# Kernel tuning notes

Hardware: AMD Instinct MI355X
Metric: run time of the kernel (lower is better)

## Reference

```python
import jax, jax.numpy as jnp
import numpy as np

B, S, V, E, H, K = 64, 512, 50000, 128, 256, 20
PAD_IDX, SOS_IDX = 0, 19
NEG = -9999.0


def _lstm_dir(x, mask, W_ih, W_hh, b):
    # x: [B,S,E], mask: [B,S] float. PyTorch gate order: i,f,g,o.
    xg = jnp.einsum('bse,ge->bsg', x, W_ih) + b  # [B,S,4H]

    def step(carry, inp):
        h, c = carry
        xg_t, m = inp  # [B,4H], [B,1]
        g = xg_t + h @ W_hh.T
        i, f, gg, o = jnp.split(g, 4, axis=-1)
        i = jax.nn.sigmoid(i); f = jax.nn.sigmoid(f); o = jax.nn.sigmoid(o)
        gg = jnp.tanh(gg)
        c_new = f * c + i * gg
        h_new = o * jnp.tanh(c_new)
        h = m * h_new + (1.0 - m) * h
        c = m * c_new + (1.0 - m) * c
        return (h, c), h * m  # packed/pad_packed => zeros at padding

    h0 = jnp.zeros((x.shape[0], W_hh.shape[1]), x.dtype)
    _, hs = jax.lax.scan(step, (h0, h0), (xg.transpose(1, 0, 2), mask.T[:, :, None]))
    return hs.transpose(1, 0, 2)  # [B,S,H]


def setup_inputs() -> dict:
    key = jax.random.key(0)
    ks = jax.random.split(key, 12)
    word_seq = jax.random.randint(ks[0], (B, S), 0, V)
    tags = jax.random.randint(ks[1], (B, S), 1, K - 1)  # avoid pad(0) and sos(K-1)
    lengths = S // 2 + jax.random.randint(ks[2], (B,), 0, S // 2)
    sc = 0.1
    embed = jax.random.normal(ks[3], (V, E), jnp.float32) * sc
    W_ih_f = jax.random.normal(ks[4], (4 * H, E), jnp.float32) * sc
    W_hh_f = jax.random.normal(ks[5], (4 * H, H), jnp.float32) * sc
    b_f = jnp.zeros((4 * H,), jnp.float32).at[H:2 * H].set(1.0)  # forget bias 1
    W_ih_b = jax.random.normal(ks[6], (4 * H, E), jnp.float32) * sc
    W_hh_b = jax.random.normal(ks[7], (4 * H, H), jnp.float32) * sc
    b_b = jnp.zeros((4 * H,), jnp.float32).at[H:2 * H].set(1.0)
    lin_W = jax.random.normal(ks[8], (K, 2 * H), jnp.float32) * sc
    lin_b = jnp.zeros((K,), jnp.float32)
    trans = jax.random.normal(ks[9], (K, K), jnp.float32) * 0.1 - 1.0
    trans = trans.at[SOS_IDX, :].set(NEG).at[:, PAD_IDX].set(NEG)
    trans = trans.at[PAD_IDX, :].set(NEG).at[PAD_IDX, PAD_IDX].set(0.0)
    return dict(word_seq=word_seq, tags=tags, lengths=lengths, embed=embed,
                W_ih_f=W_ih_f, W_hh_f=W_hh_f, b_f=b_f,
                W_ih_b=W_ih_b, W_hh_b=W_hh_b, b_b=b_b,
                lin_W=lin_W, lin_b=lin_b, trans=trans)


def reference(word_seq, tags, lengths, embed, W_ih_f, W_hh_f, b_f,
              W_ih_b, W_hh_b, b_b, lin_W, lin_b, trans):
    mask = (jnp.arange(S)[None, :] < lengths[:, None]).astype(jnp.float32)  # [B,S]
    x = embed[word_seq]  # [B,S,E]

    # forward direction
    h_f = _lstm_dir(x, mask, W_ih_f, W_hh_f, b_f)
    # backward direction: reverse within each valid length (packed-seq semantics)
    t = jnp.arange(S)[None, :]
    ri = jnp.where(t < lengths[:, None], lengths[:, None] - 1 - t, t)  # [B,S]
    x_rev = jnp.take_along_axis(x, ri[:, :, None], axis=1)
    h_b_rev = _lstm_dir(x_rev, mask, W_ih_b, W_hh_b, b_b)
    h_b = jnp.take_along_axis(h_b_rev, ri[:, :, None], axis=1)

    rnn_out = jnp.concatenate([h_f, h_b], axis=-1)  # [B,S,2H]
    feats = jnp.einsum('bsd,kd->bsk', rnn_out, lin_W) + lin_b  # [B,S,K]

    # --- CRF numerator: score of gold path ---
    states = jnp.concatenate(
        [jnp.full((B, 1), SOS_IDX, dtype=tags.dtype), tags], axis=1)  # [B,S+1]
    emis = jnp.take_along_axis(feats, tags[:, :, None], axis=-1)[..., 0]  # [B,S]
    trn = trans[states[:, 1:], states[:, :-1]]  # [B,S]
    numerator = jnp.sum((emis + trn) * mask, axis=1)  # [B]

    # --- CRF denominator: forward algorithm (log partition) ---
    score0 = jnp.full((B, K), NEG, jnp.float32).at[:, SOS_IDX].set(0.0)

    def step(score, inp):
        em, m = inp  # [B,K], [B,1]
        new = jax.nn.logsumexp(
            score[:, None, :] + em[:, :, None] + trans[None, :, :], axis=-1)
        score = m * new + (1.0 - m) * score
        return score, None

    score, _ = jax.lax.scan(
        step, score0, (feats.transpose(1, 0, 2), mask.T[:, :, None]))
    denominator = jax.nn.logsumexp(score, axis=-1)  # [B]

    return denominator - numerator  # per-example negative log-likelihood [B]
```

## Files before the change

### kernel.cpp

```cpp
#include <hip/hip_runtime.h>
#include <hip/hip_fp16.h>
#include <stdint.h>

#define BB 64
#define SS 512
#define EE 128
#define HH 256
#define KK 20
#define NEGV -9999.0f
#define SOS_IDX 19

typedef unsigned int u32;

__device__ __forceinline__ float sigm(float x){ return 1.0f / (1.0f + __expf(-x)); }
__device__ __forceinline__ float tanh_fast(float x){
  float e = __expf(2.f * x);
  return 1.f - 2.f / (e + 1.f);
}

__device__ __forceinline__ void pk4(uint4 w, const __half2* hp,
                                    __half2& a0, __half2& a1, __half2& a2, __half2& a3){
  __half2 w0 = *(__half2*)&w.x, w1 = *(__half2*)&w.y, w2 = *(__half2*)&w.z, w3 = *(__half2*)&w.w;
  a0 = __hfma2(w0, hp[0], a0);
  a1 = __hfma2(w1, hp[1], a1);
  a2 = __hfma2(w2, hp[2], a2);
  a3 = __hfma2(w3, hp[3], a3);
}
__device__ __forceinline__ float flushacc(__half2& a0, __half2& a1, __half2& a2, __half2& a3){
  float2 f0 = __half22float2(a0), f1 = __half22float2(a1);
  float2 f2 = __half22float2(a2), f3 = __half22float2(a3);
  __half2 z = __floats2half2_rn(0.f, 0.f);
  a0 = z; a1 = z; a2 = z; a3 = z;
  return ((f0.x + f0.y) + (f1.x + f1.y)) + ((f2.x + f2.y) + (f3.x + f3.y));
}

__global__ void prep_whh(const float* __restrict__ whh_f, const float* __restrict__ whh_b,
                         __half* __restrict__ wp){
  int id = blockIdx.x * 256 + threadIdx.x;
  if (id >= 524288) return;
  int d = id >> 18;
  int rem = id & 262143;
  int row = rem >> 8;
  int k = rem & 255;
  const float* w = d ? whh_b : whh_f;
  wp[(((size_t)d * 32 + (k >> 3)) * 1024 + row) * 8 + (k & 7)] = __float2half(w[row * 256 + k]);
}

__global__ void prep_wih(const float* __restrict__ wih_f, const float* __restrict__ wih_b,
                         float* __restrict__ wt){
  int id = blockIdx.x * 256 + threadIdx.x;
  if (id >= 262144) return;
  int d = id >> 17;
  int rem = id & 131071;
  int col = rem >> 7;
  int k = rem & 127;
  const float* w = d ? wih_b : wih_f;
  wt[(size_t)k * 2048 + d * 1024 + col] = w[col * 128 + k];
}

__global__ __launch_bounds__(256) void xg_gemm(const int* __restrict__ word_seq,
    const float* __restrict__ embed, const float* __restrict__ wt,
    const float* __restrict__ b_f, const float* __restrict__ b_b,
    __half* __restrict__ xg){
  __shared__ __align__(16) float xs[16][128];
  int rb = blockIdx.x >> 1, cb = blockIdx.x & 1;
  int tid = threadIdx.x;
  {
    int r = tid >> 4, kq = (tid & 15) * 8;
    int bs = rb * 16 + r;
    int w = word_seq[bs];
    const float* er = embed + (size_t)w * 128 + kq;
    float4 a = *(const float4*)er;
    float4 b = *(const float4*)(er + 4);
    *(float4*)&xs[r][kq] = a;
    *(float4*)&xs[r][kq + 4] = b;
  }
  __syncthreads();
  int co = tid * 4;
  const float* bias = cb ? b_b : b_f;
  float4 bv = *(const float4*)(bias + co);
  float4 acc[16];
  #pragma unroll
  for (int r = 0; r < 16; r++) acc[r] = bv;
  const float* wptr = wt + cb * 1024 + co;
  for (int k = 0; k < 128; k++){
    float4 w4 = *(const float4*)(wptr + (size_t)k * 2048);
    #pragma unroll
    for (int r = 0; r < 16; r++){
      float xv = xs[r][k];
      acc[r].x += xv * w4.x; acc[r].y += xv * w4.y;
      acc[r].z += xv * w4.z; acc[r].w += xv * w4.w;
    }
  }
  __half* base = xg + (size_t)cb * ((size_t)BB * SS * 1024);
  #pragma unroll
  for (int r = 0; r < 16; r++){
    int bs = rb * 16 + r;
    __half* o = base + (size_t)bs * 1024 + co;
    __half2 p0 = __floats2half2_rn(acc[r].x, acc[r].y);
    __half2 p1 = __floats2half2_rn(acc[r].z, acc[r].w);
    uint2 st; st.x = *(u32*)&p0; st.y = *(u32*)&p1;
    *(uint2*)o = st;
  }
}

__global__ __launch_bounds__(1024) void lstm_seq(const int* __restrict__ lengths,
    const __half* __restrict__ wp, const __half* __restrict__ xg,
    float* __restrict__ rnn){
  extern __shared__ __align__(16) char smem[];
  u32*     wl  = (u32*)smem;
  float*   gl  = (float*)(smem + 147456);
  __half2* hl2 = (__half2*)(smem + 151552);
  __half*  hlh = (__half*)(smem + 151552);

  int bx = blockIdx.x;
  int b = bx & 63, d = bx >> 6;
  int tid = threadIdx.x;
  int l = lengths[b];
  const uint4* wp4 = (const uint4*)(wp + (size_t)d * (32 * 1024 * 8));

  uint4 wr[6];
  #pragma unroll
  for (int c = 0; c < 6; c++) wr[c] = wp4[c * 1024 + tid];
  #pragma unroll
  for (int c = 0; c < 9; c++){
    uint4 v = wp4[(6 + c) * 1024 + tid];
    *(uint4*)&wl[(c * 1024 + tid) * 4] = v;
  }
  if (tid < 256) hlh[tid] = __float2half(0.f);
  float cc = 0.f;
  const __half* xgd = xg + ((size_t)d * BB * SS + (size_t)b * SS) * 1024;
  float* rbp = rnn + (size_t)b * SS * 512 + d * 256;
  for (int i = tid; i < (SS - l) * 256; i += 1024){
    int s = l + (i >> 8), j = i & 255;
    rbp[(size_t)s * 512 + j] = 0.f;
  }
  int gate = tid >> 8;
  const uint4* sp4 = wp4 + 15 * 1024;
  __syncthreads();

  for (int t = 0; t < l; t++){
    int s = d ? (l - 1 - t) : t;
    float xv = __half2float(xgd[(size_t)s * 1024 + tid]);
    uint4 s0[5];
    #pragma unroll
    for (int c = 0; c < 5; c++) s0[c] = sp4[c * 1024 + tid];

    __half2 z = __floats2half2_rn(0.f, 0.f);
    __half2 a0 = z, a1 = z, a2 = z, a3 = z;
    float fa;
    #pragma unroll
    for (int c = 0; c < 6; c++) pk4(wr[c], hl2 + c * 4, a0, a1, a2, a3);
    fa = flushacc(a0, a1, a2, a3);
    uint4 s1[5];
    #pragma unroll
    for (int c = 0; c < 5; c++) s1[c] = sp4[(5 + c) * 1024 + tid];
    #pragma unroll
    for (int c = 0; c < 9; c++){
      uint4 wv = *(const uint4*)&wl[(c * 1024 + tid) * 4];
      pk4(wv, hl2 + 24 + c * 4, a0, a1, a2, a3);
    }
    fa += flushacc(a0, a1, a2, a3);
    #pragma unroll
    for (int c = 0; c < 5; c++) pk4(s0[c], hl2 + 60 + c * 4, a0, a1, a2, a3);
    #pragma unroll
    for (int c = 0; c < 5; c++) s0[c] = sp4[(10 + c) * 1024 + tid];
    #pragma unroll
    for (int c = 0; c < 5; c++) pk4(s1[c], hl2 + 80 + c * 4, a0, a1, a2, a3);
    s1[0] = sp4[15 * 1024 + tid];
    s1[1] = sp4[16 * 1024 + tid];
    fa += flushacc(a0, a1, a2, a3);
    #pragma unroll
    for (int c = 0; c < 5; c++) pk4(s0[c], hl2 + 100 + c * 4, a0, a1, a2, a3);
    pk4(s1[0], hl2 + 120, a0, a1, a2, a3);
    pk4(s1[1], hl2 + 124, a0, a1, a2, a3);
    fa += flushacc(a0, a1, a2, a3);

    float a = fa + xv;
    float gv = (gate == 2) ? tanh_fast(a) : sigm(a);
    gl[tid] = gv;
    __syncthreads();
    if (tid < 256){
      float iv = gl[tid], fv = gl[tid + 256], gg = gl[tid + 512], ov = gl[tid + 768];
      cc = fv * cc + iv * gg;
      float h = ov * tanh_fast(cc);
      hlh[tid] = __float2half(h);
      rbp[(size_t)s * 512 + tid] = h;
    }
    __syncthreads();
  }
}

__global__ void feat_gemv(const float* __restrict__ rnn,
    const float* __restrict__ linW, const float* __restrict__ linb,
    float* __restrict__ feats){
  int id = blockIdx.x * 256 + threadIdx.x;
  if (id >= BB * SS * KK) return;
  int row = id / 20;
  int col = id - row * 20;
  const float* rr = rnn + (size_t)row * 512;
  const float* wr = linW + col * 512;
  float acc = linb[col];
  for (int k8 = 0; k8 < 64; k8++){
    float4 ra = *(const float4*)(rr + k8 * 8);
    float4 rb = *(const float4*)(rr + k8 * 8 + 4);
    float4 wa = *(const float4*)(wr + k8 * 8);
    float4 wb = *(const float4*)(wr + k8 * 8 + 4);
    acc += ra.x * wa.x + ra.y * wa.y + ra.z * wa.z + ra.w * wa.w
         + rb.x * wb.x + rb.y * wb.y + rb.z * wb.z + rb.w * wb.w;
  }
  feats[id] = acc;
}

__global__ __launch_bounds__(64) void crf_kernel(const int* __restrict__ tags,
    const int* __restrict__ lengths, const float* __restrict__ trans,
    const float* __restrict__ feats, float* __restrict__ out){
  int b = blockIdx.x, tid = threadIdx.x;
  __shared__ float tr[400];
  __shared__ float sc[20];
  for (int i = tid; i < 400; i += 64) tr[i] = trans[i];
  __syncthreads();
  int l = lengths[b];
  const int* tg = tags + b * SS;
  const float* fb = feats + (size_t)b * SS * 20;
  float p = 0.f;
  for (int s = tid; s < SS; s += 64){
    if (s < l){
      int cur = tg[s];
      int prev = s ? tg[s - 1] : SOS_IDX;
      p += fb[s * 20 + cur] + tr[cur * 20 + prev];
    }
  }
  #pragma unroll
  for (int off = 32; off; off >>= 1) p += __shfl_down(p, off);
  if (tid < 20) sc[tid] = (tid == SOS_IDX) ? 0.f : NEGV;
  __syncthreads();
  float em = (tid < 20 && l > 0) ? fb[tid] : 0.f;
  for (int s = 0; s < l; s++){
    float em_nxt = (tid < 20 && (s + 1) < l) ? fb[(s + 1) * 20 + tid] : 0.f;
    float nv = 0.f;
    if (tid < 20){
      const float* trow = &tr[tid * 20];
      float v[20];
      float m = -1e30f;
      #pragma unroll
      for (int jj = 0; jj < 20; jj++){ v[jj] = sc[jj] + trow[jj]; m = fmaxf(m, v[jj]); }
      float ssum = 0.f;
      #pragma unroll
      for (int jj = 0; jj < 20; jj++) ssum += __expf(v[jj] - m);
      nv = em + m + __logf(ssum);
    }
    __syncthreads();
    if (tid < 20) sc[tid] = nv;
    __syncthreads();
    em = em_nxt;
  }
  if (tid == 0){
    float m = -1e30f;
    #pragma unroll
    for (int i = 0; i < 20; i++) m = fmaxf(m, sc[i]);
    float ssum = 0.f;
    #pragma unroll
    for (int i = 0; i < 20; i++) ssum += __expf(sc[i] - m);
    out[b] = (m + __logf(ssum)) - p;
  }
}

extern "C" void kernel_launch(void* const* d_in, const int* in_sizes, int n_in,
                              void* d_out, int out_size, void* d_ws, size_t ws_size,
                              hipStream_t stream){
  const int*   word_seq = (const int*)d_in[0];
  const int*   tags     = (const int*)d_in[1];
  const int*   lengths  = (const int*)d_in[2];
  const float* embed    = (const float*)d_in[3];
  const float* wih_f    = (const float*)d_in[4];
  const float* whh_f    = (const float*)d_in[5];
  const float* b_f      = (const float*)d_in[6];
  const float* wih_b    = (const float*)d_in[7];
  const float* whh_b    = (const float*)d_in[8];
  const float* b_b      = (const float*)d_in[9];
  const float* linW     = (const float*)d_in[10];
  const float* linb     = (const float*)d_in[11];
  const float* trans    = (const float*)d_in[12];
  float* out = (float*)d_out;

  char* ws = (char*)d_ws;
  __half* wp    = (__half*)ws;
  float*  wt    = (float*)(ws + (1ull << 20));
  __half* xg    = (__half*)(ws + (2ull << 20));
  float*  rnn   = (float*)(ws + (2ull << 20) + (128ull << 20));
  float*  feats = (float*)(ws + (2ull << 20) + (192ull << 20));

  (void)hipFuncSetAttribute((const void*)lstm_seq,
        hipFuncAttributeMaxDynamicSharedMemorySize, 152064);

  prep_whh<<<dim3(2048), dim3(256), 0, stream>>>(whh_f, whh_b, wp);
  prep_wih<<<dim3(1024), dim3(256), 0, stream>>>(wih_f, wih_b, wt);
  xg_gemm<<<dim3(4096), dim3(256), 0, stream>>>(word_seq, embed, wt, b_f, b_b, xg);
  lstm_seq<<<dim3(128), dim3(1024), 152064, stream>>>(lengths, wp, xg, rnn);
  feat_gemv<<<dim3(2560), dim3(256), 0, stream>>>(rnn, linW, linb, feats);
  crf_kernel<<<dim3(64), dim3(64), 0, stream>>>(tags, lengths, trans, feats, out);
}
```

Measured before the change: 1.776 ms.

## Restructure LSTM recurrence to 256 threads each computing all four gates

The recurrent kernel moves from 1024 threads (one gate row each) to 256 threads, where each thread computes the i,f,g,o rows for one hidden unit. This removes the shared-memory gate exchange and one of the two barriers per timestep, and double-buffers the hidden state. Weight placement changes so that 16 chunks per gate sit in registers (256 VGPRs of weights), 8 sit in LDS and 8 stream from global memory. The risks are very high register pressure with possible spills, and four times more serial FMA work per thread on the latency-bound critical path.

```diff
diff --git a/kernel.cpp b/kernel.cpp
--- a/kernel.cpp
+++ b/kernel.cpp
@@ -104,14 +104,12 @@
   }
 }
 
-__global__ __launch_bounds__(1024) void lstm_seq(const int* __restrict__ lengths,
+__global__ __launch_bounds__(256, 1) void lstm_seq(const int* __restrict__ lengths,
     const __half* __restrict__ wp, const __half* __restrict__ xg,
     float* __restrict__ rnn){
   extern __shared__ __align__(16) char smem[];
-  u32*     wl  = (u32*)smem;
-  float*   gl  = (float*)(smem + 147456);
-  __half2* hl2 = (__half2*)(smem + 151552);
-  __half*  hlh = (__half*)(smem + 151552);
+  u32*    wl = (u32*)smem;
+  __half* hb = (__half*)(smem + 131072);
 
   int bx = blockIdx.x;
   int b = bx & 63, d = bx >> 6;
@@ -119,75 +117,138 @@
   int l = lengths[b];
   const uint4* wp4 = (const uint4*)(wp + (size_t)d * (32 * 1024 * 8));
 
-  uint4 wr[6];
-  #pragma unroll
-  for (int c = 0; c < 6; c++) wr[c] = wp4[c * 1024 + tid];
-  #pragma unroll
-  for (int c = 0; c < 9; c++){
-    uint4 v = wp4[(6 + c) * 1024 + tid];
-    *(uint4*)&wl[(c * 1024 + tid) * 4] = v;
-  }
-  if (tid < 256) hlh[tid] = __float2half(0.f);
+  uint4 wr[4][16];
+  #pragma unroll
+  for (int g = 0; g < 4; g++){
+    int row = tid + g * 256;
+    #pragma unroll
+    for (int c = 0; c < 16; c++) wr[g][c] = wp4[c * 1024 + row];
+  }
+  #pragma unroll
+  for (int g = 0; g < 4; g++){
+    int row = tid + g * 256;
+    #pragma unroll
+    for (int c = 0; c < 8; c++){
+      uint4 v = wp4[(16 + c) * 1024 + row];
+      *(uint4*)&wl[((g * 8 + c) * 256 + tid) * 4] = v;
+    }
+  }
+  hb[tid] = __float2half(0.f);
   float cc = 0.f;
   const __half* xgd = xg + ((size_t)d * BB * SS + (size_t)b * SS) * 1024;
   float* rbp = rnn + (size_t)b * SS * 512 + d * 256;
-  for (int i = tid; i < (SS - l) * 256; i += 1024){
-    int s = l + (i >> 8), j = i & 255;
-    rbp[(size_t)s * 512 + j] = 0.f;
-  }
-  int gate = tid >> 8;
-  const uint4* sp4 = wp4 + 15 * 1024;
+  for (int s = l; s < SS; s++) rbp[(size_t)s * 512 + tid] = 0.f;
+  int cur = 0;
   __syncthreads();
 
   for (int t = 0; t < l; t++){
     int s = d ? (l - 1 - t) : t;
-    float xv = __half2float(xgd[(size_t)s * 1024 + tid]);
-    uint4 s0[5];
-    #pragma unroll
-    for (int c = 0; c < 5; c++) s0[c] = sp4[c * 1024 + tid];
-
+    const __half* xr = xgd + (size_t)s * 1024 + tid;
+    float xv0 = __half2float(xr[0]);
+    float xv1 = __half2float(xr[256]);
+    float xv2 = __half2float(xr[512]);
+    float xv3 = __half2float(xr[768]);
+    const __half* hc = &hb[cur * 256];
+    uint4 sA[4][2], sB[4][2];
+    #pragma unroll
+    for (int g = 0; g < 4; g++){
+      int row = tid + g * 256;
+      sA[g][0] = wp4[24 * 1024 + row];
+      sA[g][1] = wp4[25 * 1024 + row];
+      sB[g][0] = wp4[26 * 1024 + row];
+      sB[g][1] = wp4[27 * 1024 + row];
+    }
     __half2 z = __floats2half2_rn(0.f, 0.f);
-    __half2 a0 = z, a1 = z, a2 = z, a3 = z;
-    float fa;
-    #pragma unroll
-    for (int c = 0; c < 6; c++) pk4(wr[c], hl2 + c * 4, a0, a1, a2, a3);
-    fa = flushacc(a0, a1, a2, a3);
-    uint4 s1[5];
-    #pragma unroll
-    for (int c = 0; c < 5; c++) s1[c] = sp4[(5 + c) * 1024 + tid];
-    #pragma unroll
-    for (int c = 0; c < 9; c++){
-      uint4 wv = *(const uint4*)&wl[(c * 1024 + tid) * 4];
-      pk4(wv, hl2 + 24 + c * 4, a0, a1, a2, a3);
-    }
-    fa += flushacc(a0, a1, a2, a3);
-    #pragma unroll
-    for (int c = 0; c < 5; c++) pk4(s0[c], hl2 + 60 + c * 4, a0, a1, a2, a3);
-    #pragma unroll
-    for (int c = 0; c < 5; c++) s0[c] = sp4[(10 + c) * 1024 + tid];
-    #pragma unroll
-    for (int c = 0; c < 5; c++) pk4(s1[c], hl2 + 80 + c * 4, a0, a1, a2, a3);
-    s1[0] = sp4[15 * 1024 + tid];
-    s1[1] = sp4[16 * 1024 + tid];
-    fa += flushacc(a0, a1, a2, a3);
-    #pragma unroll
-    for (int c = 0; c < 5; c++) pk4(s0[c], hl2 + 100 + c * 4, a0, a1, a2, a3);
-    pk4(s1[0], hl2 + 120, a0, a1, a2, a3);
-    pk4(s1[1], hl2 + 124, a0, a1, a2, a3);
-    fa += flushacc(a0, a1, a2, a3);
-
-    float a = fa + xv;
-    float gv = (gate == 2) ? tanh_fast(a) : sigm(a);
-    gl[tid] = gv;
+    __half2 acc[4][4];
+    #pragma unroll
+    for (int g = 0; g < 4; g++){
+      acc[g][0] = z; acc[g][1] = z; acc[g][2] = z; acc[g][3] = z;
+    }
+    float fa[4];
+    #pragma unroll
+    for (int c = 0; c < 16; c++){
+      uint4 hv = *(const uint4*)&hc[c * 8];
+      const __half2* hp = (const __half2*)&hv;
+      #pragma unroll
+      for (int g = 0; g < 4; g++) pk4(wr[g][c], hp, acc[g][0], acc[g][1], acc[g][2], acc[g][3]);
+    }
+    #pragma unroll
+    for (int g = 0; g < 4; g++) fa[g] = flushacc(acc[g][0], acc[g][1], acc[g][2], acc[g][3]);
+    #pragma unroll
+    for (int c = 0; c < 8; c++){
+      uint4 hv = *(const uint4*)&hc[(16 + c) * 8];
+      const __half2* hp = (const __half2*)&hv;
+      #pragma unroll
+      for (int g = 0; g < 4; g++){
+        uint4 wv = *(const uint4*)&wl[((g * 8 + c) * 256 + tid) * 4];
+        pk4(wv, hp, acc[g][0], acc[g][1], acc[g][2], acc[g][3]);
+      }
+    }
+    #pragma unroll
+    for (int g = 0; g < 4; g++) fa[g] += flushacc(acc[g][0], acc[g][1], acc[g][2], acc[g][3]);
+    {
+      uint4 hv = *(const uint4*)&hc[24 * 8];
+      const __half2* hp = (const __half2*)&hv;
+      #pragma unroll
+      for (int g = 0; g < 4; g++) pk4(sA[g][0], hp, acc[g][0], acc[g][1], acc[g][2], acc[g][3]);
+      uint4 hv2 = *(const uint4*)&hc[25 * 8];
+      const __half2* hp2 = (const __half2*)&hv2;
+      #pragma unroll
+      for (int g = 0; g < 4; g++) pk4(sA[g][1], hp2, acc[g][0], acc[g][1], acc[g][2], acc[g][3]);
+    }
+    #pragma unroll
+    for (int g = 0; g < 4; g++){
+      int row = tid + g * 256;
+      sA[g][0] = wp4[28 * 1024 + row];
+      sA[g][1] = wp4[29 * 1024 + row];
+    }
+    {
+      uint4 hv = *(const uint4*)&hc[26 * 8];
+      const __half2* hp = (const __half2*)&hv;
+      #pragma unroll
+      for (int g = 0; g < 4; g++) pk4(sB[g][0], hp, acc[g][0], acc[g][1], acc[g][2], acc[g][3]);
+      uint4 hv2 = *(const uint4*)&hc[27 * 8];
+      const __half2* hp2 = (const __half2*)&hv2;
+      #pragma unroll
+      for (int g = 0; g < 4; g++) pk4(sB[g][1], hp2, acc[g][0], acc[g][1], acc[g][2], acc[g][3]);
+    }
+    #pragma unroll
+    for (int g = 0; g < 4; g++){
+      int row = tid + g * 256;
+      sB[g][0] = wp4[30 * 1024 + row];
+      sB[g][1] = wp4[31 * 1024 + row];
+    }
+    {
+      uint4 hv = *(const uint4*)&hc[28 * 8];
+      const __half2* hp = (const __half2*)&hv;
+      #pragma unroll
+      for (int g = 0; g < 4; g++) pk4(sA[g][0], hp, acc[g][0], acc[g][1], acc[g][2], acc[g][3]);
+      uint4 hv2 = *(const uint4*)&hc[29 * 8];
+      const __half2* hp2 = (const __half2*)&hv2;
+      #pragma unroll
+      for (int g = 0; g < 4; g++) pk4(sA[g][1], hp2, acc[g][0], acc[g][1], acc[g][2], acc[g][3]);
+      uint4 hv3 = *(const uint4*)&hc[30 * 8];
+      const __half2* hp3 = (const __half2*)&hv3;
+      #pragma unroll
+      for (int g = 0; g < 4; g++) pk4(sB[g][0], hp3, acc[g][0], acc[g][1], acc[g][2], acc[g][3]);
+      uint4 hv4 = *(const uint4*)&hc[31 * 8];
+      const __half2* hp4 = (const __half2*)&hv4;
+      #pragma unroll
+      for (int g = 0; g < 4; g++) pk4(sB[g][1], hp4, acc[g][0], acc[g][1], acc[g][2], acc[g][3]);
+    }
+    #pragma unroll
+    for (int g = 0; g < 4; g++) fa[g] += flushacc(acc[g][0], acc[g][1], acc[g][2], acc[g][3]);
+
+    float iv = sigm(fa[0] + xv0);
+    float fv = sigm(fa[1] + xv1);
+    float gv = tanh_fast(fa[2] + xv2);
+    float ov = sigm(fa[3] + xv3);
+    cc = fv * cc + iv * gv;
+    float h = ov * tanh_fast(cc);
+    hb[(cur ^ 1) * 256 + tid] = __float2half(h);
+    rbp[(size_t)s * 512 + tid] = h;
     __syncthreads();
-    if (tid < 256){
-      float iv = gl[tid], fv = gl[tid + 256], gg = gl[tid + 512], ov = gl[tid + 768];
-      cc = fv * cc + iv * gg;
-      float h = ov * tanh_fast(cc);
-      hlh[tid] = __float2half(h);
-      rbp[(size_t)s * 512 + tid] = h;
-    }
-    __syncthreads();
+    cur ^= 1;
   }
 }
 
@@ -292,12 +353,12 @@
   float*  feats = (float*)(ws + (2ull << 20) + (192ull << 20));
 
   (void)hipFuncSetAttribute((const void*)lstm_seq,
-        hipFuncAttributeMaxDynamicSharedMemorySize, 152064);
+        hipFuncAttributeMaxDynamicSharedMemorySize, 132096);
 
   prep_whh<<<dim3(2048), dim3(256), 0, stream>>>(whh_f, whh_b, wp);
   prep_wih<<<dim3(1024), dim3(256), 0, stream>>>(wih_f, wih_b, wt);
   xg_gemm<<<dim3(4096), dim3(256), 0, stream>>>(word_seq, embed, wt, b_f, b_b, xg);
-  lstm_seq<<<dim3(128), dim3(1024), 152064, stream>>>(lengths, wp, xg, rnn);
+  lstm_seq<<<dim3(128), dim3(256), 132096, stream>>>(lengths, wp, xg, rnn);
   feat_gemv<<<dim3(2560), dim3(256), 0, stream>>>(rnn, linW, linb, feats);
   crf_kernel<<<dim3(64), dim3(64), 0, stream>>>(tags, lengths, trans, feats, out);
 }
```

Result: slower. 2.801 ms (+57.7%).

## Compute two gate rows per thread with shuffle-based cell update in LSTM

Applied to the files above, without the earlier changes.

The LSTM recurrence kernel now runs 512 threads, each computing two gate rows. A thread pair holds all four gates of one hidden unit, so the cell update is done with lane shuffles instead of a shared-memory gate buffer and a second barrier. The tanh gate is computed through a scaled sigmoid. The hidden state is double-buffered to allow one barrier per step, and more weights are kept in registers with the rest in LDS and global. This raises register pressure, with a risk of spills, and relies on the hardware's fp16 dot arithmetic staying the same.

```diff
diff --git a/kernel.cpp b/kernel.cpp
--- a/kernel.cpp
+++ b/kernel.cpp
@@ -104,90 +104,106 @@
   }
 }
 
-__global__ __launch_bounds__(1024) void lstm_seq(const int* __restrict__ lengths,
+__global__ __launch_bounds__(512, 2) void lstm_seq(const int* __restrict__ lengths,
     const __half* __restrict__ wp, const __half* __restrict__ xg,
     float* __restrict__ rnn){
   extern __shared__ __align__(16) char smem[];
-  u32*     wl  = (u32*)smem;
-  float*   gl  = (float*)(smem + 147456);
-  __half2* hl2 = (__half2*)(smem + 151552);
-  __half*  hlh = (__half*)(smem + 151552);
+  u32*    wl = (u32*)smem;
+  __half* hb = (__half*)(smem + 147456);
 
   int bx = blockIdx.x;
   int b = bx & 63, d = bx >> 6;
   int tid = threadIdx.x;
+  int u = tid >> 1, q = tid & 1;
+  int row0 = u + q * 256;
+  int row1 = row0 + 512;
   int l = lengths[b];
   const uint4* wp4 = (const uint4*)(wp + (size_t)d * (32 * 1024 * 8));
 
-  uint4 wr[6];
-  #pragma unroll
-  for (int c = 0; c < 6; c++) wr[c] = wp4[c * 1024 + tid];
+  uint4 wr0[17], wr1[17];
+  #pragma unroll
+  for (int c = 0; c < 17; c++){ wr0[c] = wp4[c * 1024 + row0]; wr1[c] = wp4[c * 1024 + row1]; }
   #pragma unroll
   for (int c = 0; c < 9; c++){
-    uint4 v = wp4[(6 + c) * 1024 + tid];
-    *(uint4*)&wl[(c * 1024 + tid) * 4] = v;
-  }
-  if (tid < 256) hlh[tid] = __float2half(0.f);
+    *(uint4*)&wl[((c * 2 + 0) * 512 + tid) * 4] = wp4[(17 + c) * 1024 + row0];
+    *(uint4*)&wl[((c * 2 + 1) * 512 + tid) * 4] = wp4[(17 + c) * 1024 + row1];
+  }
+  if (tid < 256) hb[tid] = __float2half(0.f);
   float cc = 0.f;
   const __half* xgd = xg + ((size_t)d * BB * SS + (size_t)b * SS) * 1024;
   float* rbp = rnn + (size_t)b * SS * 512 + d * 256;
-  for (int i = tid; i < (SS - l) * 256; i += 1024){
+  for (int i = tid; i < (SS - l) * 256; i += 512){
     int s = l + (i >> 8), j = i & 255;
     rbp[(size_t)s * 512 + j] = 0.f;
   }
-  int gate = tid >> 8;
-  const uint4* sp4 = wp4 + 15 * 1024;
+  float nsc = q ? 1.f : 2.f;
+  float nmu = q ? 1.f : 2.f;
+  float nad = q ? 0.f : -1.f;
+  int cur = 0;
   __syncthreads();
 
   for (int t = 0; t < l; t++){
     int s = d ? (l - 1 - t) : t;
-    float xv = __half2float(xgd[(size_t)s * 1024 + tid]);
-    uint4 s0[5];
-    #pragma unroll
-    for (int c = 0; c < 5; c++) s0[c] = sp4[c * 1024 + tid];
-
+    const __half* xr = xgd + (size_t)s * 1024;
+    float xv0 = __half2float(xr[row0]);
+    float xv1 = __half2float(xr[row1]);
+    uint4 s0[6], s1[6];
+    #pragma unroll
+    for (int c = 0; c < 6; c++){
+      s0[c] = wp4[(26 + c) * 1024 + row0];
+      s1[c] = wp4[(26 + c) * 1024 + row1];
+    }
+    const __half* hc = &hb[cur * 256];
     __half2 z = __floats2half2_rn(0.f, 0.f);
-    __half2 a0 = z, a1 = z, a2 = z, a3 = z;
-    float fa;
-    #pragma unroll
-    for (int c = 0; c < 6; c++) pk4(wr[c], hl2 + c * 4, a0, a1, a2, a3);
-    fa = flushacc(a0, a1, a2, a3);
-    uint4 s1[5];
-    #pragma unroll
-    for (int c = 0; c < 5; c++) s1[c] = sp4[(5 + c) * 1024 + tid];
+    __half2 a00 = z, a01 = z, a02 = z, a03 = z;
+    __half2 a10 = z, a11 = z, a12 = z, a13 = z;
+    float fa0, fa1;
+    #pragma unroll
+    for (int c = 0; c < 17; c++){
+      uint4 hv = *(const uint4*)&hc[c * 8];
+      const __half2* hp = (const __half2*)&hv;
+      pk4(wr0[c], hp, a00, a01, a02, a03);
+      pk4(wr1[c], hp, a10, a11, a12, a13);
+    }
+    fa0 = flushacc(a00, a01, a02, a03);
+    fa1 = flushacc(a10, a11, a12, a13);
     #pragma unroll
     for (int c = 0; c < 9; c++){
-      uint4 wv = *(const uint4*)&wl[(c * 1024 + tid) * 4];
-      pk4(wv, hl2 + 24 + c * 4, a0, a1, a2, a3);
-    }
-    fa += flushacc(a0, a1, a2, a3);
-    #pragma unroll
-    for (int c = 0; c < 5; c++) pk4(s0[c], hl2 + 60 + c * 4, a0, a1, a2, a3);
-    #pragma unroll
-    for (int c = 0; c < 5; c++) s0[c] = sp4[(10 + c) * 1024 + tid];
-    #pragma unroll
-    for (int c = 0; c < 5; c++) pk4(s1[c], hl2 + 80 + c * 4, a0, a1, a2, a3);
-    s1[0] = sp4[15 * 1024 + tid];
-    s1[1] = sp4[16 * 1024 + tid];
-    fa += flushacc(a0, a1, a2, a3);
-    #pragma unroll
-    for (int c = 0; c < 5; c++) pk4(s0[c], hl2 + 100 + c * 4, a0, a1, a2, a3);
-    pk4(s1[0], hl2 + 120, a0, a1, a2, a3);
-    pk4(s1[1], hl2 + 124, a0, a1, a2, a3);
-    fa += flushacc(a0, a1, a2, a3);
-
-    float a = fa + xv;
-    float gv = (gate == 2) ? tanh_fast(a) : sigm(a);
-    gl[tid] = gv;
+      uint4 hv = *(const uint4*)&hc[(17 + c) * 8];
+      const __half2* hp = (const __half2*)&hv;
+      uint4 w0 = *(const uint4*)&wl[((c * 2 + 0) * 512 + tid) * 4];
+      uint4 w1 = *(const uint4*)&wl[((c * 2 + 1) * 512 + tid) * 4];
+      pk4(w0, hp, a00, a01, a02, a03);
+      pk4(w1, hp, a10, a11, a12, a13);
+    }
+    fa0 += flushacc(a00, a01, a02, a03);
+    fa1 += flushacc(a10, a11, a12, a13);
+    #pragma unroll
+    for (int c = 0; c < 6; c++){
+      uint4 hv = *(const uint4*)&hc[(26 + c) * 8];
+      const __half2* hp = (const __half2*)&hv;
+      pk4(s0[c], hp, a00, a01, a02, a03);
+      pk4(s1[c], hp, a10, a11, a12, a13);
+    }
+    fa0 += flushacc(a00, a01, a02, a03);
+    fa1 += flushacc(a10, a11, a12, a13);
+
+    fa0 += xv0;
+    fa1 += xv1;
+    float g0 = sigm(fa0);
+    float g1 = sigm(nsc * fa1) * nmu + nad;
+    float p0 = __shfl_xor(g0, 1);
+    float p1 = __shfl_xor(g1, 1);
+    float iv = q ? p0 : g0;
+    float fv = q ? g0 : p0;
+    float gv = q ? p1 : g1;
+    float ov = q ? g1 : p1;
+    cc = fv * cc + iv * gv;
+    float h = ov * tanh_fast(cc);
+    if (q) rbp[(size_t)s * 512 + u] = h;
+    else   hb[(cur ^ 1) * 256 + u] = __float2half(h);
     __syncthreads();
-    if (tid < 256){
-      float iv = gl[tid], fv = gl[tid + 256], gg = gl[tid + 512], ov = gl[tid + 768];
-      cc = fv * cc + iv * gg;
-      float h = ov * tanh_fast(cc);
-      hlh[tid] = __float2half(h);
-      rbp[(size_t)s * 512 + tid] = h;
-    }
-    __syncthreads();
+    cur ^= 1;
   }
 }
 
@@ -292,12 +308,12 @@
   float*  feats = (float*)(ws + (2ull << 20) + (192ull << 20));
 
   (void)hipFuncSetAttribute((const void*)lstm_seq,
-        hipFuncAttributeMaxDynamicSharedMemorySize, 152064);
+        hipFuncAttributeMaxDynamicSharedMemorySize, 148480);
 
   prep_whh<<<dim3(2048), dim3(256), 0, stream>>>(whh_f, whh_b, wp);
   prep_wih<<<dim3(1024), dim3(256), 0, stream>>>(wih_f, wih_b, wt);
   xg_gemm<<<dim3(4096), dim3(256), 0, stream>>>(word_seq, embed, wt, b_f, b_b, xg);
-  lstm_seq<<<dim3(128), dim3(1024), 152064, stream>>>(lengths, wp, xg, rnn);
+  lstm_seq<<<dim3(128), dim3(512), 148480, stream>>>(lengths, wp, xg, rnn);
   feat_gemv<<<dim3(2560), dim3(256), 0, stream>>>(rnn, linW, linb, feats);
   crf_kernel<<<dim3(64), dim3(64), 0, stream>>>(tags, lengths, trans, feats, out);
 }
```

New measurement: 1.631 ms. 1.09x faster.
